# Kernel optimization log

Hardware: AMD Instinct MI355X
Metric: run time of the kernel (lower is better)

## Reference

```python
import jax, jax.numpy as jnp
import numpy as np


def setup_inputs() -> dict:
    key = jax.random.key(0)
    k1, k2, k3, k4 = jax.random.split(key, 4)
    B, S, K, N = 4, 2048, 4096, 4096
    # int8-valued quantized activations / weights (held in int32 containers)
    a = jax.random.randint(k1, (B, S, K), -128, 128, dtype=jnp.int32)
    w = jax.random.randint(k2, (K, N), -128, 128, dtype=jnp.int32)
    # per-token activation scale and per-output-column weight scale
    a_scale = jax.random.uniform(k3, (B, S, 1), dtype=jnp.float32) * 0.01
    w_scale = jax.random.uniform(k4, (1, N), dtype=jnp.float32) * 0.01
    return {"a": a, "a_scale": a_scale, "w": w, "w_scale": w_scale}


def reference(a, a_scale, w, w_scale):
    # int8 GEMM with int32 accumulation (torch._int_mm equivalent),
    # batched over B instead of a per-slice Python loop.
    acc = jnp.einsum("bsk,kn->bsn", a, w)  # int32 accumulate
    # dequant epilogue: out = acc * (a_scale * w_scale), then cast to model dtype
    out = acc.astype(jnp.float32) * (a_scale * w_scale)  # [B,S,N]
    return out.astype(jnp.float32)
```

## Files before the change

### kernel.cpp

```cpp
#include <hip/hip_runtime.h>


#define M_TOT 8192
#define N_TOT 4096
#define K_TOT 4096
#define NT_K  (K_TOT / 64)
#define TILE_BYTES 16384

typedef int v4i  __attribute__((ext_vector_type(4)));
typedef int v16i __attribute__((ext_vector_type(16)));

typedef const __attribute__((address_space(1))) unsigned char* gas1_t;
typedef __attribute__((address_space(3))) unsigned char* las3_t;

__device__ __forceinline__ int pack4(int4 v) {
    return (int)((unsigned)(v.x & 255) | ((unsigned)(v.y & 255) << 8) |
                 ((unsigned)(v.z & 255) << 16) | ((unsigned)v.w << 24));
}

__global__ __launch_bounds__(256) void pack_a_kernel(const int* __restrict__ a,
                                                     unsigned char* __restrict__ a8) {
    __shared__ int4 stage[256 * 16];
    const int tile = blockIdx.x;
    const int kt = tile & (NT_K - 1);
    const int mt = tile >> 6;
    const int t = threadIdx.x;
#pragma unroll
    for (int i = 0; i < 16; ++i) {
        const int idx16 = i * 256 + t;
        const int r = idx16 >> 4;
        const int c = idx16 & 15;
        int4 v = *(const int4*)(a + (size_t)(mt * 256 + r) * K_TOT + kt * 64 + c * 4);
        stage[r * 16 + (c ^ (r & 15))] = v;
    }
    __syncthreads();
    unsigned char* outp = a8 + (size_t)tile * TILE_BYTES;
#pragma unroll
    for (int j = 0; j < 4; ++j) {
        int4 d0 = stage[t * 16 + ((j * 4 + 0) ^ (t & 15))];
        int4 d1 = stage[t * 16 + ((j * 4 + 1) ^ (t & 15))];
        int4 d2 = stage[t * 16 + ((j * 4 + 2) ^ (t & 15))];
        int4 d3 = stage[t * 16 + ((j * 4 + 3) ^ (t & 15))];
        int4 p = { pack4(d0), pack4(d1), pack4(d2), pack4(d3) };
        *(int4*)(outp + j * 4096 + t * 16) = p;
    }
}

__global__ __launch_bounds__(256) void pack_w_kernel(const int* __restrict__ w,
                                                     unsigned char* __restrict__ w8) {
    __shared__ int stage[64 * 256];
    const int tile = blockIdx.x;
    const int kt = tile & (NT_K - 1);
    const int nt = tile >> 6;
    const int t = threadIdx.x;
#pragma unroll
    for (int i = 0; i < 16; ++i) {
        const int idx = i * 256 + t;
        const int k = idx >> 6;
        const int c4 = idx & 63;
        int4 v = *(const int4*)(w + (size_t)(kt * 64 + k) * N_TOT + nt * 256 + c4 * 4);
        *(int4*)&stage[k * 256 + c4 * 4] = v;
    }
    __syncthreads();
    unsigned char* outp = w8 + (size_t)tile * TILE_BYTES;
#pragma unroll
    for (int j = 0; j < 4; ++j) {
        int4 p;
#pragma unroll
        for (int qq = 0; qq < 4; ++qq) {
            int4 b;
            b.x = stage[(j * 16 + qq * 4 + 0) * 256 + t];
            b.y = stage[(j * 16 + qq * 4 + 1) * 256 + t];
            b.z = stage[(j * 16 + qq * 4 + 2) * 256 + t];
            b.w = stage[(j * 16 + qq * 4 + 3) * 256 + t];
            ((int*)&p)[qq] = pack4(b);
        }
        *(int4*)(outp + j * 4096 + t * 16) = p;
    }
}

__global__ __launch_bounds__(512, 2) void gemm_i8_kernel(
    const unsigned char* __restrict__ a8, const unsigned char* __restrict__ w8,
    const float* __restrict__ a_scale, const float* __restrict__ w_scale,
    float* __restrict__ out) {

    __shared__ __attribute__((aligned(16))) unsigned char sm[3][2][TILE_BYTES];

    const int t = threadIdx.x;
    const int lane = t & 63;
    const int wid = t >> 6;
    const int wr = wid >> 2;
    const int wc = wid & 3;
    const int hi = lane >> 5;
    const int lo32 = lane & 31;

    int bid = blockIdx.x;
    bid = (bid & 7) * (512 / 8) + (bid >> 3);
    const int mt = bid >> 4;
    const int nt = bid & 15;

    const unsigned char* a_tiles = a8 + (size_t)mt * NT_K * TILE_BYTES;
    const unsigned char* w_tiles = w8 + (size_t)nt * NT_K * TILE_BYTES;

    v16i acc[4][2] = {};

#define STAGE_TILE(b2, gaP, gbP) do {                                             \
    __builtin_amdgcn_global_load_lds((gas1_t)((gaP) + t * 16),                    \
        (las3_t)&sm[b2][0][t * 16], 16, 0, 0);                                    \
    __builtin_amdgcn_global_load_lds((gas1_t)((gaP) + 8192 + t * 16),             \
        (las3_t)&sm[b2][0][8192 + t * 16], 16, 0, 0);                             \
    __builtin_amdgcn_global_load_lds((gas1_t)((gbP) + t * 16),                    \
        (las3_t)&sm[b2][1][t * 16], 16, 0, 0);                                    \
    __builtin_amdgcn_global_load_lds((gas1_t)((gbP) + 8192 + t * 16),             \
        (las3_t)&sm[b2][1][8192 + t * 16], 16, 0, 0);                             \
} while (0)

#define ITER(b0, b2, Tcur) do {                                                   \
    const int Tp = ((Tcur) + 2 <= NT_K - 1) ? (Tcur) + 2 : NT_K - 1;              \
    STAGE_TILE(b2, a_tiles + (size_t)Tp * TILE_BYTES,                             \
                   w_tiles + (size_t)Tp * TILE_BYTES);                            \
    v4i af[2][4], bf[2][2];                                                       \
    const unsigned char* lA = &sm[b0][0][0];                                      \
    const unsigned char* lB = &sm[b0][1][0];                                      \
    _Pragma("unroll")                                                             \
    for (int kc = 0; kc < 2; ++kc) {                                              \
        const int so = (kc * 2 + hi) * 4096;                                      \
        _Pragma("unroll")                                                         \
        for (int mi = 0; mi < 4; ++mi)                                            \
            af[kc][mi] = *(const v4i*)(lA + so + (wr * 128 + mi * 32 + lo32) * 16);\
        _Pragma("unroll")                                                         \
        for (int ni = 0; ni < 2; ++ni)                                            \
            bf[kc][ni] = *(const v4i*)(lB + so + (wc * 64 + ni * 32 + lo32) * 16);\
    }                                                                             \
    asm volatile("s_waitcnt vmcnt(4)" ::: "memory");                              \
    __builtin_amdgcn_s_barrier();                                                 \
    asm volatile("s_waitcnt lgkmcnt(0)" ::: "memory");                            \
    __builtin_amdgcn_sched_barrier(0);                                            \
    __builtin_amdgcn_s_setprio(1);                                                \
    _Pragma("unroll")                                                             \
    for (int kc = 0; kc < 2; ++kc)                                                \
        _Pragma("unroll")                                                         \
        for (int mi = 0; mi < 4; ++mi)                                            \
            _Pragma("unroll")                                                     \
            for (int ni = 0; ni < 2; ++ni)                                        \
                acc[mi][ni] = __builtin_amdgcn_mfma_i32_32x32x32_i8(              \
                    af[kc][mi], bf[kc][ni], acc[mi][ni], 0, 0, 0);                \
    __builtin_amdgcn_s_setprio(0);                                                \
    __builtin_amdgcn_s_barrier();                                                 \
} while (0)

    STAGE_TILE(0, a_tiles, w_tiles);
    STAGE_TILE(1, a_tiles + TILE_BYTES, w_tiles + TILE_BYTES);
    asm volatile("s_waitcnt vmcnt(4)" ::: "memory");
    __builtin_amdgcn_s_barrier();

    int T = 0;
#pragma unroll 1
    for (int u = 0; u < 21; ++u) {
        ITER(0, 2, T);
        ITER(1, 0, T + 1);
        ITER(2, 1, T + 2);
        T += 3;
    }
    ITER(0, 2, 63);

    asm volatile("s_waitcnt vmcnt(0)" ::: "memory");

#undef STAGE_TILE
#undef ITER

    const int row0 = mt * 256 + wr * 128;
    const int col0 = nt * 256 + wc * 64;
#pragma unroll
    for (int mi = 0; mi < 4; ++mi) {
#pragma unroll
        for (int r = 0; r < 16; ++r) {
            const int row = row0 + mi * 32 + (r & 3) + 8 * (r >> 2) + 4 * hi;
            const float as = a_scale[row];
            float* orow = out + (size_t)row * N_TOT + col0 + lo32;
#pragma unroll
            for (int ni = 0; ni < 2; ++ni)
                orow[ni * 32] = (float)acc[mi][ni][r] * as * w_scale[col0 + ni * 32 + lo32];
        }
    }
}

extern "C" void kernel_launch(void* const* d_in, const int* in_sizes, int n_in,
                              void* d_out, int out_size, void* d_ws, size_t ws_size,
                              hipStream_t stream) {
    const int*   a       = (const int*)d_in[0];
    const float* a_scale = (const float*)d_in[1];
    const int*   w       = (const int*)d_in[2];
    const float* w_scale = (const float*)d_in[3];
    float*       out     = (float*)d_out;

    unsigned char* a8 = (unsigned char*)d_ws;
    unsigned char* w8 = a8 + (size_t)M_TOT * K_TOT;

    pack_a_kernel<<<(M_TOT / 256) * NT_K, 256, 0, stream>>>(a, a8);
    pack_w_kernel<<<(N_TOT / 256) * NT_K, 256, 0, stream>>>(w, w8);
    gemm_i8_kernel<<<(M_TOT / 256) * (N_TOT / 256), 512, 0, stream>>>(
        a8, w8, a_scale, w_scale, out);
}
```

Measured before the change: 402.3 us.

## Deepen GEMM LDS pipeline to four stages, split fragment loads, cache scales

```diff
diff --git a/kernel.cpp b/kernel.cpp
--- a/kernel.cpp
+++ b/kernel.cpp
@@ -20,62 +20,74 @@
 
 __global__ __launch_bounds__(256) void pack_a_kernel(const int* __restrict__ a,
                                                      unsigned char* __restrict__ a8) {
-    __shared__ int4 stage[256 * 16];
-    const int tile = blockIdx.x;
-    const int kt = tile & (NT_K - 1);
-    const int mt = tile >> 6;
+    __shared__ int4 stage[128 * 16];
+    const int b = blockIdx.x;
+    const int kt = b & (NT_K - 1);
+    const int m128 = b >> 6;
+    const int mt = m128 >> 1;
+    const int mhalf = m128 & 1;
     const int t = threadIdx.x;
 #pragma unroll
-    for (int i = 0; i < 16; ++i) {
+    for (int i = 0; i < 8; ++i) {
         const int idx16 = i * 256 + t;
         const int r = idx16 >> 4;
         const int c = idx16 & 15;
-        int4 v = *(const int4*)(a + (size_t)(mt * 256 + r) * K_TOT + kt * 64 + c * 4);
+        int4 v = *(const int4*)(a + (size_t)(mt * 256 + mhalf * 128 + r) * K_TOT +
+                                kt * 64 + c * 4);
         stage[r * 16 + (c ^ (r & 15))] = v;
     }
     __syncthreads();
-    unsigned char* outp = a8 + (size_t)tile * TILE_BYTES;
-#pragma unroll
-    for (int j = 0; j < 4; ++j) {
-        int4 d0 = stage[t * 16 + ((j * 4 + 0) ^ (t & 15))];
-        int4 d1 = stage[t * 16 + ((j * 4 + 1) ^ (t & 15))];
-        int4 d2 = stage[t * 16 + ((j * 4 + 2) ^ (t & 15))];
-        int4 d3 = stage[t * 16 + ((j * 4 + 3) ^ (t & 15))];
+    unsigned char* outp = a8 + (size_t)(mt * NT_K + kt) * TILE_BYTES;
+#pragma unroll
+    for (int q = 0; q < 2; ++q) {
+        const int id = q * 256 + t;
+        const int j = id >> 7;
+        const int r = id & 127;
+        int4 d0 = stage[r * 16 + ((j * 4 + 0) ^ (r & 15))];
+        int4 d1 = stage[r * 16 + ((j * 4 + 1) ^ (r & 15))];
+        int4 d2 = stage[r * 16 + ((j * 4 + 2) ^ (r & 15))];
+        int4 d3 = stage[r * 16 + ((j * 4 + 3) ^ (r & 15))];
         int4 p = { pack4(d0), pack4(d1), pack4(d2), pack4(d3) };
-        *(int4*)(outp + j * 4096 + t * 16) = p;
+        *(int4*)(outp + j * 4096 + (mhalf * 128 + r) * 16) = p;
     }
 }
 
 __global__ __launch_bounds__(256) void pack_w_kernel(const int* __restrict__ w,
                                                      unsigned char* __restrict__ w8) {
-    __shared__ int stage[64 * 256];
-    const int tile = blockIdx.x;
-    const int kt = tile & (NT_K - 1);
-    const int nt = tile >> 6;
+    __shared__ int stage[64 * 128];
+    const int b = blockIdx.x;
+    const int kt = b & (NT_K - 1);
+    const int n128 = b >> 6;
+    const int nt = n128 >> 1;
+    const int nhalf = n128 & 1;
     const int t = threadIdx.x;
 #pragma unroll
-    for (int i = 0; i < 16; ++i) {
+    for (int i = 0; i < 8; ++i) {
         const int idx = i * 256 + t;
-        const int k = idx >> 6;
-        const int c4 = idx & 63;
-        int4 v = *(const int4*)(w + (size_t)(kt * 64 + k) * N_TOT + nt * 256 + c4 * 4);
-        *(int4*)&stage[k * 256 + c4 * 4] = v;
-    }
-    __syncthreads();
-    unsigned char* outp = w8 + (size_t)tile * TILE_BYTES;
-#pragma unroll
-    for (int j = 0; j < 4; ++j) {
+        const int k = idx >> 5;
+        const int c4 = idx & 31;
+        int4 v = *(const int4*)(w + (size_t)(kt * 64 + k) * N_TOT +
+                                nt * 256 + nhalf * 128 + c4 * 4);
+        *(int4*)&stage[k * 128 + c4 * 4] = v;
+    }
+    __syncthreads();
+    unsigned char* outp = w8 + (size_t)(nt * NT_K + kt) * TILE_BYTES;
+#pragma unroll
+    for (int q = 0; q < 2; ++q) {
+        const int id = q * 256 + t;
+        const int j = id >> 7;
+        const int n = id & 127;
         int4 p;
 #pragma unroll
         for (int qq = 0; qq < 4; ++qq) {
-            int4 b;
-            b.x = stage[(j * 16 + qq * 4 + 0) * 256 + t];
-            b.y = stage[(j * 16 + qq * 4 + 1) * 256 + t];
-            b.z = stage[(j * 16 + qq * 4 + 2) * 256 + t];
-            b.w = stage[(j * 16 + qq * 4 + 3) * 256 + t];
-            ((int*)&p)[qq] = pack4(b);
+            int4 bb;
+            bb.x = stage[(j * 16 + qq * 4 + 0) * 128 + n];
+            bb.y = stage[(j * 16 + qq * 4 + 1) * 128 + n];
+            bb.z = stage[(j * 16 + qq * 4 + 2) * 128 + n];
+            bb.w = stage[(j * 16 + qq * 4 + 3) * 128 + n];
+            ((int*)&p)[qq] = pack4(bb);
         }
-        *(int4*)(outp + j * 4096 + t * 16) = p;
+        *(int4*)(outp + j * 4096 + (nhalf * 128 + n) * 16) = p;
     }
 }
 
@@ -84,7 +96,7 @@
     const float* __restrict__ a_scale, const float* __restrict__ w_scale,
     float* __restrict__ out) {
 
-    __shared__ __attribute__((aligned(16))) unsigned char sm[3][2][TILE_BYTES];
+    __shared__ __attribute__((aligned(16))) unsigned char sm[4][2][TILE_BYTES];
 
     const int t = threadIdx.x;
     const int lane = t & 63;
@@ -104,85 +116,103 @@
 
     v16i acc[4][2] = {};
 
-#define STAGE_TILE(b2, gaP, gbP) do {                                             \
+#define STAGE_TILE(bN, gaP, gbP) do {                                             \
     __builtin_amdgcn_global_load_lds((gas1_t)((gaP) + t * 16),                    \
-        (las3_t)&sm[b2][0][t * 16], 16, 0, 0);                                    \
+        (las3_t)&sm[bN][0][t * 16], 16, 0, 0);                                    \
     __builtin_amdgcn_global_load_lds((gas1_t)((gaP) + 8192 + t * 16),             \
-        (las3_t)&sm[b2][0][8192 + t * 16], 16, 0, 0);                             \
+        (las3_t)&sm[bN][0][8192 + t * 16], 16, 0, 0);                             \
     __builtin_amdgcn_global_load_lds((gas1_t)((gbP) + t * 16),                    \
-        (las3_t)&sm[b2][1][t * 16], 16, 0, 0);                                    \
+        (las3_t)&sm[bN][1][t * 16], 16, 0, 0);                                    \
     __builtin_amdgcn_global_load_lds((gas1_t)((gbP) + 8192 + t * 16),             \
-        (las3_t)&sm[b2][1][8192 + t * 16], 16, 0, 0);                             \
+        (las3_t)&sm[bN][1][8192 + t * 16], 16, 0, 0);                             \
 } while (0)
 
-#define ITER(b0, b2, Tcur) do {                                                   \
-    const int Tp = ((Tcur) + 2 <= NT_K - 1) ? (Tcur) + 2 : NT_K - 1;              \
-    STAGE_TILE(b2, a_tiles + (size_t)Tp * TILE_BYTES,                             \
+#define ITER(b0, b3, Tcur) do {                                                   \
+    const int Tp = ((Tcur) + 3 <= NT_K - 1) ? (Tcur) + 3 : NT_K - 1;              \
+    STAGE_TILE(b3, a_tiles + (size_t)Tp * TILE_BYTES,                             \
                    w_tiles + (size_t)Tp * TILE_BYTES);                            \
-    v4i af[2][4], bf[2][2];                                                       \
     const unsigned char* lA = &sm[b0][0][0];                                      \
     const unsigned char* lB = &sm[b0][1][0];                                      \
-    _Pragma("unroll")                                                             \
-    for (int kc = 0; kc < 2; ++kc) {                                              \
-        const int so = (kc * 2 + hi) * 4096;                                      \
-        _Pragma("unroll")                                                         \
-        for (int mi = 0; mi < 4; ++mi)                                            \
-            af[kc][mi] = *(const v4i*)(lA + so + (wr * 128 + mi * 32 + lo32) * 16);\
+    v4i af0[4], bf0[2], af1[4], bf1[2];                                           \
+    _Pragma("unroll")                                                             \
+    for (int mi = 0; mi < 4; ++mi)                                                \
+        af0[mi] = *(const v4i*)(lA + hi * 4096 + (wr * 128 + mi * 32 + lo32) * 16);\
+    _Pragma("unroll")                                                             \
+    for (int ni = 0; ni < 2; ++ni)                                                \
+        bf0[ni] = *(const v4i*)(lB + hi * 4096 + (wc * 64 + ni * 32 + lo32) * 16);\
+    __builtin_amdgcn_sched_barrier(0);   \
+    _Pragma("unroll")                                                             \
+    for (int mi = 0; mi < 4; ++mi)                                                \
+        af1[mi] = *(const v4i*)(lA + (2 + hi) * 4096 + (wr * 128 + mi * 32 + lo32) * 16);\
+    _Pragma("unroll")                                                             \
+    for (int ni = 0; ni < 2; ++ni)                                                \
+        bf1[ni] = *(const v4i*)(lB + (2 + hi) * 4096 + (wc * 64 + ni * 32 + lo32) * 16);\
+    asm volatile("s_waitcnt vmcnt(8)" ::: "memory");                              \
+    __builtin_amdgcn_s_barrier();                                                 \
+    asm volatile("s_waitcnt lgkmcnt(6)" ::: "memory");                            \
+    __builtin_amdgcn_sched_barrier(0);                                            \
+    __builtin_amdgcn_s_setprio(1);                                                \
+    _Pragma("unroll")                                                             \
+    for (int mi = 0; mi < 4; ++mi)                                                \
         _Pragma("unroll")                                                         \
         for (int ni = 0; ni < 2; ++ni)                                            \
-            bf[kc][ni] = *(const v4i*)(lB + so + (wc * 64 + ni * 32 + lo32) * 16);\
-    }                                                                             \
-    asm volatile("s_waitcnt vmcnt(4)" ::: "memory");                              \
-    __builtin_amdgcn_s_barrier();                                                 \
+            acc[mi][ni] = __builtin_amdgcn_mfma_i32_32x32x32_i8(                  \
+                af0[mi], bf0[ni], acc[mi][ni], 0, 0, 0);                          \
     asm volatile("s_waitcnt lgkmcnt(0)" ::: "memory");                            \
     __builtin_amdgcn_sched_barrier(0);                                            \
-    __builtin_amdgcn_s_setprio(1);                                                \
-    _Pragma("unroll")                                                             \
-    for (int kc = 0; kc < 2; ++kc)                                                \
+    _Pragma("unroll")                                                             \
+    for (int mi = 0; mi < 4; ++mi)                                                \
         _Pragma("unroll")                                                         \
-        for (int mi = 0; mi < 4; ++mi)                                            \
-            _Pragma("unroll")                                                     \
-            for (int ni = 0; ni < 2; ++ni)                                        \
-                acc[mi][ni] = __builtin_amdgcn_mfma_i32_32x32x32_i8(              \
-                    af[kc][mi], bf[kc][ni], acc[mi][ni], 0, 0, 0);                \
+        for (int ni = 0; ni < 2; ++ni)                                            \
+            acc[mi][ni] = __builtin_amdgcn_mfma_i32_32x32x32_i8(                  \
+                af1[mi], bf1[ni], acc[mi][ni], 0, 0, 0);                          \
     __builtin_amdgcn_s_setprio(0);                                                \
     __builtin_amdgcn_s_barrier();                                                 \
 } while (0)
 
     STAGE_TILE(0, a_tiles, w_tiles);
     STAGE_TILE(1, a_tiles + TILE_BYTES, w_tiles + TILE_BYTES);
-    asm volatile("s_waitcnt vmcnt(4)" ::: "memory");
+    STAGE_TILE(2, a_tiles + 2 * TILE_BYTES, w_tiles + 2 * TILE_BYTES);
+    asm volatile("s_waitcnt vmcnt(8)" ::: "memory");
     __builtin_amdgcn_s_barrier();
 
     int T = 0;
 #pragma unroll 1
-    for (int u = 0; u < 21; ++u) {
-        ITER(0, 2, T);
+    for (int u = 0; u < 16; ++u) {
+        ITER(0, 3, T);
         ITER(1, 0, T + 1);
         ITER(2, 1, T + 2);
-        T += 3;
-    }
-    ITER(0, 2, 63);
+        ITER(3, 2, T + 3);
+        T += 4;
+    }
 
     asm volatile("s_waitcnt vmcnt(0)" ::: "memory");
 
 #undef STAGE_TILE
 #undef ITER
 
+    __syncthreads();
+    float* scA = (float*)&sm[0][0][0];
+    float* scW = scA + 256;
+    if (t < 256) scA[t] = a_scale[mt * 256 + t];
+    else         scW[t - 256] = w_scale[nt * 256 + (t - 256)];
+    __syncthreads();
+
     const int row0 = mt * 256 + wr * 128;
     const int col0 = nt * 256 + wc * 64;
 #pragma unroll
     for (int mi = 0; mi < 4; ++mi) {
 #pragma unroll
         for (int r = 0; r < 16; ++r) {
-            const int row = row0 + mi * 32 + (r & 3) + 8 * (r >> 2) + 4 * hi;
-            const float as = a_scale[row];
-            float* orow = out + (size_t)row * N_TOT + col0 + lo32;
+            const int rloc = wr * 128 + mi * 32 + (r & 3) + 8 * (r >> 2) + 4 * hi;
+            const float as = scA[rloc];
+            float* orow = out + (size_t)(row0 - wr * 128 + rloc) * N_TOT + col0 + lo32;
 #pragma unroll
             for (int ni = 0; ni < 2; ++ni)
-                orow[ni * 32] = (float)acc[mi][ni][r] * as * w_scale[col0 + ni * 32 + lo32];
+                orow[ni * 32] = (float)acc[mi][ni][r] * as * scW[wc * 64 + ni * 32 + lo32];
         }
     }
+    (void)row0;
 }
 
 extern "C" void kernel_launch(void* const* d_in, const int* in_sizes, int n_in,
@@ -197,8 +227,8 @@
     unsigned char* a8 = (unsigned char*)d_ws;
     unsigned char* w8 = a8 + (size_t)M_TOT * K_TOT;
 
-    pack_a_kernel<<<(M_TOT / 256) * NT_K, 256, 0, stream>>>(a, a8);
-    pack_w_kernel<<<(N_TOT / 256) * NT_K, 256, 0, stream>>>(w, w8);
+    pack_a_kernel<<<(M_TOT / 128) * NT_K, 256, 0, stream>>>(a, a8);
+    pack_w_kernel<<<(N_TOT / 128) * NT_K, 256, 0, stream>>>(w, w8);
     gemm_i8_kernel<<<(M_TOT / 256) * (N_TOT / 256), 512, 0, stream>>>(
         a8, w8, a_scale, w_scale, out);
 }
```

After: 397.0 us. About the same (-1.3%).
